# Performance work log

Measured on AMD Instinct MI355X. Metric: run time of the kernel, lower is better.

## Reference

```python
import jax, jax.numpy as jnp
import numpy as np

B, D, C, H = 65536, 256, 128, 1024
SPLIT = D // 2           # transformed half (odd indices under 'even' mask)
NET_IN = (D - SPLIT) + C # unchanged half + cond


def setup_inputs() -> dict:
    key = jax.random.key(0)
    ks = jax.random.split(key, 10)
    s = 0.02
    return {
        "x": jax.random.normal(ks[0], (B, D), jnp.float32),
        "cond": jax.random.normal(ks[1], (B, C), jnp.float32),
        "W1": jax.random.normal(ks[2], (NET_IN, H), jnp.float32) * s,
        "b1": jnp.zeros((H,), jnp.float32),
        "W2": jax.random.normal(ks[3], (H, H), jnp.float32) * s,
        "b2": jnp.zeros((H,), jnp.float32),
        "Ws": jax.random.normal(ks[4], (H, SPLIT), jnp.float32) * s,
        "bs": jnp.zeros((SPLIT,), jnp.float32),
        "Wt": jax.random.normal(ks[5], (H, SPLIT), jnp.float32) * s,
        "bt": jnp.zeros((SPLIT,), jnp.float32),
    }


def reference(x, cond, W1, b1, W2, b2, Ws, bs, Wt, bt):
    d = x.shape[1]
    even = jnp.arange(0, d, 2)  # mask==1 -> unchanged (x1)
    odd = jnp.arange(1, d, 2)   # mask==0 -> transformed (x2)
    x1u = x[:, even]            # (B, d - d//2)
    x2u = x[:, odd]             # (B, d//2)
    h = jax.nn.relu(jnp.concatenate([x1u, cond], axis=1) @ W1 + b1)
    h = jax.nn.relu(h @ W2 + b2)
    log_s = jnp.tanh(h @ Ws + bs)
    t = h @ Wt + bt
    x2t = x2u * jnp.exp(log_s) + t
    out = jnp.zeros_like(x).at[:, even].set(x1u).at[:, odd].set(x2t)
    log_det = jnp.sum(log_s, axis=1)
    return out, log_det
```

## Files before the change

kernel.cpp:

```cpp
#include <hip/hip_runtime.h>
#include <hip/hip_bf16.h>
#include <math.h>

#define B_ROWS 65536
#define D_DIM 256
#define C_DIM 128
#define H_DIM 1024

typedef __bf16 bf16x8 __attribute__((ext_vector_type(8)));
typedef float f32x4 __attribute__((ext_vector_type(4)));
typedef short short8 __attribute__((ext_vector_type(8)));

__device__ __forceinline__ unsigned short f2bf(float f) {
    unsigned int u = __float_as_uint(f);
    u += 0x7fffu + ((u >> 16) & 1u);
    return (unsigned short)(u >> 16);
}

__device__ __forceinline__ void gl2lds16(const void* g, void* l) {
    __builtin_amdgcn_global_load_lds(
        (const __attribute__((address_space(1))) unsigned int*)g,
        (__attribute__((address_space(3))) unsigned int*)l, 16, 0, 0);
}

__device__ __forceinline__ void swizzle_mn(int id, int mtiles, int& m, int& n) {
    if ((mtiles & 7) == 0) {
        int g = id >> 6, r = id & 63;
        m = g * 8 + (r & 7);
        n = r >> 3;
    } else {
        m = id >> 3;
        n = id & 7;
    }
}

__global__ void transpose_bf16(const float* __restrict__ src, short* __restrict__ dst,
                               int R, int C, int total) {
    int tid = blockIdx.x * 256 + threadIdx.x;
    if (tid >= total) return;
    int per = R >> 3;
    int n = tid / per;
    int k0 = (tid - n * per) << 3;
    short8 o;
#pragma unroll
    for (int j = 0; j < 8; ++j) o[j] = (short)f2bf(src[(size_t)(k0 + j) * C + n]);
    *(short8*)&dst[(size_t)n * R + k0] = o;
}

__global__ void prep_b3(const float* __restrict__ bs, const float* __restrict__ bt,
                        float* __restrict__ b3) {
    int i = threadIdx.x;
    b3[i] = (i < 128) ? bs[i] : bt[i - 128];
}

__global__ __launch_bounds__(256) void gemm1_fused(
    const float* __restrict__ x, const float* __restrict__ cond,
    const short* __restrict__ Bw, const float* __restrict__ bias,
    unsigned short* __restrict__ H1, int mtiles) {
    constexpr int BK = 64, K = 256, N = 1024;
    __shared__ __align__(16) short As[128 * BK];
    __shared__ __align__(16) short Bs[128 * BK];
    const int tid = threadIdx.x;
    const int lane = tid & 63;
    const int wave = tid >> 6;
    int mt, nt;
    swizzle_mn(blockIdx.x, mtiles, mt, nt);
    const int tm = mt * 128, tn = nt * 128;
    const int mo = (wave >> 1) * 64;
    const int no = (wave & 1) * 64;

    f32x4 acc[4][4];
#pragma unroll
    for (int i = 0; i < 4; ++i)
#pragma unroll
        for (int j = 0; j < 4; ++j) acc[i][j] = f32x4{0.f, 0.f, 0.f, 0.f};

    const int srow = lane >> 3;
    const int skb = (lane & 7) ^ srow;

#pragma unroll
    for (int kc = 0; kc < K; kc += BK) {
        __syncthreads();
#pragma unroll
        for (int i = 0; i < 4; ++i) {
            int c = wave * 4 + i;
            int row = c * 8 + srow;
            int kcol = kc + skb * 8;
            float v[8];
            if (kc < 128) {
                const float4* p = (const float4*)(x + (size_t)(tm + row) * 256 + 2 * kcol);
                float4 a = p[0], b = p[1], cc = p[2], d = p[3];
                v[0]=a.x; v[1]=a.z; v[2]=b.x; v[3]=b.z; v[4]=cc.x; v[5]=cc.z; v[6]=d.x; v[7]=d.z;
            } else {
                const float4* p = (const float4*)(cond + (size_t)(tm + row) * 128 + (kcol - 128));
                float4 a = p[0], b = p[1];
                v[0]=a.x; v[1]=a.y; v[2]=a.z; v[3]=a.w; v[4]=b.x; v[5]=b.y; v[6]=b.z; v[7]=b.w;
            }
            short8 o;
#pragma unroll
            for (int j = 0; j < 8; ++j) o[j] = (short)f2bf(v[j]);
            *(short8*)&As[c * 512 + lane * 8] = o;
            gl2lds16(Bw + (size_t)(tn + row) * K + kc + skb * 8, &Bs[c * 512]);
        }
        __syncthreads();
#pragma unroll
        for (int kk = 0; kk < 2; ++kk) {
            bf16x8 af[4], bfr[4];
            int kb = kk * 4 + (lane >> 4);
#pragma unroll
            for (int t = 0; t < 4; ++t) {
                int r = mo + t * 16 + (lane & 15);
                af[t] = *(const bf16x8*)&As[r * BK + ((kb ^ (r & 7)) << 3)];
                int n = no + t * 16 + (lane & 15);
                bfr[t] = *(const bf16x8*)&Bs[n * BK + ((kb ^ (n & 7)) << 3)];
            }
#pragma unroll
            for (int i = 0; i < 4; ++i)
#pragma unroll
                for (int j = 0; j < 4; ++j)
                    acc[i][j] = __builtin_amdgcn_mfma_f32_16x16x32_bf16(
                        af[i], bfr[j], acc[i][j], 0, 0, 0);
        }
    }

#pragma unroll
    for (int j = 0; j < 4; ++j) {
        int col = tn + no + j * 16 + (lane & 15);
        float bb = bias[col];
#pragma unroll
        for (int i = 0; i < 4; ++i) {
            int row0 = tm + mo + i * 16 + ((lane >> 4) << 2);
            f32x4 v = acc[i][j];
#pragma unroll
            for (int rr = 0; rr < 4; ++rr)
                H1[(size_t)(row0 + rr) * N + col] = f2bf(fmaxf(v[rr] + bb, 0.f));
        }
    }
}

__global__ __launch_bounds__(256) void gemm_tn(
    const short* __restrict__ A, const short* __restrict__ Bw,
    const float* __restrict__ bias, unsigned short* __restrict__ Cout,
    int mtiles, int N, int K) {
    constexpr int BK = 64;
    __shared__ __align__(16) short As[128 * BK];
    __shared__ __align__(16) short Bs[128 * BK];
    const int tid = threadIdx.x;
    const int lane = tid & 63;
    const int wave = tid >> 6;
    int mt, nt;
    swizzle_mn(blockIdx.x, mtiles, mt, nt);
    const int tm = mt * 128, tn = nt * 128;
    const int mo = (wave >> 1) * 64;
    const int no = (wave & 1) * 64;

    f32x4 acc[4][4];
#pragma unroll
    for (int i = 0; i < 4; ++i)
#pragma unroll
        for (int j = 0; j < 4; ++j) acc[i][j] = f32x4{0.f, 0.f, 0.f, 0.f};

    const int srow = lane >> 3;
    const int skb = (lane & 7) ^ srow;

    for (int kc = 0; kc < K; kc += BK) {
        __syncthreads();
#pragma unroll
        for (int i = 0; i < 4; ++i) {
            int c = wave * 4 + i;
            int row = c * 8 + srow;
            gl2lds16(A + (size_t)(tm + row) * K + kc + skb * 8, &As[c * 512]);
            gl2lds16(Bw + (size_t)(tn + row) * K + kc + skb * 8, &Bs[c * 512]);
        }
        __syncthreads();
#pragma unroll
        for (int kk = 0; kk < 2; ++kk) {
            bf16x8 af[4], bfr[4];
            int kb = kk * 4 + (lane >> 4);
#pragma unroll
            for (int t = 0; t < 4; ++t) {
                int r = mo + t * 16 + (lane & 15);
                af[t] = *(const bf16x8*)&As[r * BK + ((kb ^ (r & 7)) << 3)];
                int n = no + t * 16 + (lane & 15);
                bfr[t] = *(const bf16x8*)&Bs[n * BK + ((kb ^ (n & 7)) << 3)];
            }
#pragma unroll
            for (int i = 0; i < 4; ++i)
#pragma unroll
                for (int j = 0; j < 4; ++j)
                    acc[i][j] = __builtin_amdgcn_mfma_f32_16x16x32_bf16(
                        af[i], bfr[j], acc[i][j], 0, 0, 0);
        }
    }

#pragma unroll
    for (int j = 0; j < 4; ++j) {
        int col = tn + no + j * 16 + (lane & 15);
        float bb = bias[col];
#pragma unroll
        for (int i = 0; i < 4; ++i) {
            int row0 = tm + mo + i * 16 + ((lane >> 4) << 2);
            f32x4 v = acc[i][j];
#pragma unroll
            for (int rr = 0; rr < 4; ++rr)
                Cout[(size_t)(row0 + rr) * N + col] = f2bf(fmaxf(v[rr] + bb, 0.f));
        }
    }
}

__global__ __launch_bounds__(512, 2) void gemm2_8ph(
    const short* __restrict__ A, const short* __restrict__ Bw,
    const float* __restrict__ bias, unsigned short* __restrict__ Cout) {
    constexpr int K = 1024, N = 1024, NT = 16;
    __shared__ __align__(16) short As0[256 * 64];
    __shared__ __align__(16) short Bs0[256 * 64];
    __shared__ __align__(16) short As1[256 * 64];
    __shared__ __align__(16) short Bs1[256 * 64];

    const int tid = threadIdx.x;
    const int lane = tid & 63;
    const int wave = tid >> 6;
    const int wm = wave >> 2;
    const int wn = wave & 3;
    const int l15 = lane & 15;
    const int quad = lane >> 4;
    const int srow = lane >> 3;
    const int skb8 = ((lane & 7) ^ srow) << 3;

    const int id = blockIdx.x, nwg = gridDim.x;
    const int xcd = id & 7, lid = id >> 3;
    const int q = nwg >> 3, r = nwg & 7;
    const int wgid = (xcd < r ? xcd * (q + 1) : r * (q + 1) + (xcd - r) * q) + lid;
    const int mt = wgid >> 2, nt = wgid & 3;
    const size_t Abase = (size_t)(mt * 256) * K;
    const size_t Bbase = (size_t)(nt * 256) * K;

    f32x4 acc[8][4];
#pragma unroll
    for (int m = 0; m < 8; ++m)
#pragma unroll
        for (int n = 0; n < 4; ++n) acc[m][n] = f32x4{0.f, 0.f, 0.f, 0.f};

    short *Ac = As0, *Bc = Bs0, *An = As1, *Bn = Bs1;

    auto stage2 = [&](short* lds, const short* g, size_t rowbase, int kc, int c0, int c1) {
        gl2lds16(g + rowbase + (size_t)(c0 * 8 + srow) * K + kc + skb8, &lds[c0 * 512]);
        gl2lds16(g + rowbase + (size_t)(c1 * 8 + srow) * K + kc + skb8, &lds[c1 * 512]);
    };
    auto stageU = [&](int u, short* Ab, short* Bb, int kc) {
        if (u == 0)      stage2(Bb, Bw, Bbase, kc, wave * 2, wave * 2 + 1);
        else if (u == 1) stage2(Bb, Bw, Bbase, kc, 16 + wave * 2, 17 + wave * 2);
        else if (u == 2) stage2(Ab, A, Abase, kc, wave, 16 + wave);
        else             stage2(Ab, A, Abase, kc, 8 + wave, 24 + wave);
    };

    stageU(0, Ac, Bc, 0);
    stageU(1, Ac, Bc, 0);
    stageU(2, Ac, Bc, 0);
    stageU(3, Ac, Bc, 0);
    stageU(0, An, Bn, 64);
    stageU(1, An, Bn, 64);
    stageU(2, An, Bn, 64);
    asm volatile("s_waitcnt vmcnt(6)" ::: "memory");
    __builtin_amdgcn_sched_barrier(0);
    __builtin_amdgcn_s_barrier();

    for (int w = 0; w < NT; ++w) {
        const int kc1 = (w + 1) << 6, kc2 = (w + 2) << 6;
        bf16x8 bfr[4][2], af[2][2];

#pragma unroll
        for (int n = 0; n < 4; ++n) {
            int rB = (wn << 6) + n * 16 + l15;
#pragma unroll
            for (int kk = 0; kk < 2; ++kk) {
                int kb = kk * 4 + quad;
                bfr[n][kk] = *(const bf16x8*)&Bc[rB * 64 + ((kb ^ (rB & 7)) << 3)];
            }
        }
#pragma unroll
        for (int mm = 0; mm < 2; ++mm) {
            int rA = (wm << 7) + mm * 16 + l15;
#pragma unroll
            for (int kk = 0; kk < 2; ++kk) {
                int kb = kk * 4 + quad;
                af[mm][kk] = *(const bf16x8*)&Ac[rA * 64 + ((kb ^ (rA & 7)) << 3)];
            }
        }
        if (w + 1 < NT) stageU(3, An, Bn, kc1);
        __builtin_amdgcn_sched_barrier(0);
        __builtin_amdgcn_s_barrier();
        __builtin_amdgcn_sched_barrier(0);
        __builtin_amdgcn_s_setprio(1);
#pragma unroll
        for (int kk = 0; kk < 2; ++kk)
#pragma unroll
            for (int mm = 0; mm < 2; ++mm)
#pragma unroll
                for (int n = 0; n < 4; ++n)
                    acc[mm][n] = __builtin_amdgcn_mfma_f32_16x16x32_bf16(
                        af[mm][kk], bfr[n][kk], acc[mm][n], 0, 0, 0);
        __builtin_amdgcn_s_setprio(0);
        __builtin_amdgcn_sched_barrier(0);
        __builtin_amdgcn_s_barrier();

#pragma unroll
        for (int ph = 1; ph < 4; ++ph) {
#pragma unroll
            for (int mm = 0; mm < 2; ++mm) {
                int rA = (wm << 7) + (ph * 2 + mm) * 16 + l15;
#pragma unroll
                for (int kk = 0; kk < 2; ++kk) {
                    int kb = kk * 4 + quad;
                    af[mm][kk] = *(const bf16x8*)&Ac[rA * 64 + ((kb ^ (rA & 7)) << 3)];
                }
            }
            if (w + 2 < NT) stageU(ph - 1, Ac, Bc, kc2);
            __builtin_amdgcn_sched_barrier(0);
            __builtin_amdgcn_s_barrier();
            __builtin_amdgcn_sched_barrier(0);
            __builtin_amdgcn_s_setprio(1);
#pragma unroll
            for (int kk = 0; kk < 2; ++kk)
#pragma unroll
                for (int mm = 0; mm < 2; ++mm)
#pragma unroll
                    for (int n = 0; n < 4; ++n)
                        acc[ph * 2 + mm][n] = __builtin_amdgcn_mfma_f32_16x16x32_bf16(
                            af[mm][kk], bfr[n][kk], acc[ph * 2 + mm][n], 0, 0, 0);
            __builtin_amdgcn_s_setprio(0);
            if (ph == 3) {
                if (w < NT - 2)
                    asm volatile("s_waitcnt vmcnt(6)" ::: "memory");
                else
                    asm volatile("s_waitcnt vmcnt(0)" ::: "memory");
            }
            __builtin_amdgcn_sched_barrier(0);
            __builtin_amdgcn_s_barrier();
        }

        short* t0 = Ac; Ac = An; An = t0;
        short* t1 = Bc; Bc = Bn; Bn = t1;
    }

    const int tmg = mt * 256 + (wm << 7);
    const int tng = nt * 256 + (wn << 6);
#pragma unroll
    for (int n = 0; n < 4; ++n) {
        int col = tng + n * 16 + l15;
        float bb = bias[col];
#pragma unroll
        for (int m = 0; m < 8; ++m) {
            int row0 = tmg + m * 16 + (quad << 2);
            f32x4 v = acc[m][n];
#pragma unroll
            for (int rr = 0; rr < 4; ++rr)
                Cout[(size_t)(row0 + rr) * N + col] = f2bf(fmaxf(v[rr] + bb, 0.f));
        }
    }
}

__global__ __launch_bounds__(256) void gemm3_final(
    const short* __restrict__ H2, const short* __restrict__ W3T,
    const float* __restrict__ b3, const float* __restrict__ x,
    float* __restrict__ out, float* __restrict__ logdet) {
    constexpr int BK = 64, K = 1024;
    __shared__ __align__(16) char raw[40960];
    __shared__ float rowsum[64];
    short* As = (short*)raw;
    short* Bs = (short*)(raw + 8192);
    float* Tbuf = (float*)raw;
    const int tid = threadIdx.x;
    const int lane = tid & 63;
    const int wave = tid >> 6;
    const int tm = blockIdx.x * 64;
    const int srow = lane >> 3;
    const int skb = (lane & 7) ^ srow;
    const int l15 = lane & 15;
    const int quad = lane >> 4;

    if (tid < 64) rowsum[tid] = 0.f;

    f32x4 acc[4][4];
#pragma unroll
    for (int i = 0; i < 4; ++i)
#pragma unroll
        for (int j = 0; j < 4; ++j) acc[i][j] = f32x4{0.f, 0.f, 0.f, 0.f};

    for (int kc = 0; kc < K; kc += BK) {
        __syncthreads();
#pragma unroll
        for (int i = 0; i < 10; ++i) {
            int c = wave * 10 + i;
            if (c < 8) {
                int row = c * 8 + srow;
                gl2lds16(H2 + (size_t)(tm + row) * K + kc + skb * 8, &As[c * 512]);
            } else {
                int row = (c - 8) * 8 + srow;
                gl2lds16(W3T + (size_t)row * K + kc + skb * 8, &Bs[(c - 8) * 512]);
            }
        }
        __syncthreads();
#pragma unroll
        for (int kk = 0; kk < 2; ++kk) {
            int kb = kk * 4 + quad;
            bf16x8 af[4], bfr[4];
#pragma unroll
            for (int mt = 0; mt < 4; ++mt) {
                int r = mt * 16 + l15;
                af[mt] = *(const bf16x8*)&As[r * BK + ((kb ^ (r & 7)) << 3)];
            }
#pragma unroll
            for (int nt = 0; nt < 4; ++nt) {
                int n = wave * 64 + nt * 16 + l15;
                bfr[nt] = *(const bf16x8*)&Bs[n * BK + ((kb ^ (n & 7)) << 3)];
            }
#pragma unroll
            for (int mt = 0; mt < 4; ++mt)
#pragma unroll
                for (int nt = 0; nt < 4; ++nt)
                    acc[mt][nt] = __builtin_amdgcn_mfma_f32_16x16x32_bf16(
                        af[mt], bfr[nt], acc[mt][nt], 0, 0, 0);
        }
    }

    __syncthreads();
    if (wave >= 2) {
#pragma unroll
        for (int nt = 0; nt < 4; ++nt) {
            int col = wave * 64 + nt * 16 + l15;
            float bb = b3[col];
            int cl = col - 128;
#pragma unroll
            for (int mt = 0; mt < 4; ++mt) {
#pragma unroll
                for (int rr = 0; rr < 4; ++rr) {
                    int m = mt * 16 + quad * 4 + rr;
                    Tbuf[m * 132 + cl] = acc[mt][nt][rr] + bb;
                }
            }
        }
    }
    __syncthreads();
    if (wave < 2) {
#pragma unroll
        for (int mt = 0; mt < 4; ++mt) {
#pragma unroll
            for (int rr = 0; rr < 4; ++rr) {
                int m = mt * 16 + quad * 4 + rr;
                int grow = tm + m;
                float s = 0.f;
#pragma unroll
                for (int nt = 0; nt < 4; ++nt) {
                    int j = wave * 64 + nt * 16 + l15;
                    float p = acc[mt][nt][rr] + b3[j];
                    p = fminf(fmaxf(p, -15.f), 15.f);
                    float e2 = __expf(2.f * p);
                    float ls = (e2 - 1.f) / (e2 + 1.f);
                    s += ls;
                    float tt = Tbuf[m * 132 + j];
                    float2 xv = *(const float2*)&x[(size_t)grow * 256 + 2 * j];
                    float2 ov;
                    ov.x = xv.x;
                    ov.y = xv.y * __expf(ls) + tt;
                    *(float2*)&out[(size_t)grow * 256 + 2 * j] = ov;
                }
                s += __shfl_xor(s, 1);
                s += __shfl_xor(s, 2);
                s += __shfl_xor(s, 4);
                s += __shfl_xor(s, 8);
                if (l15 == 0) atomicAdd(&rowsum[m], s);
            }
        }
    }
    __syncthreads();
    if (tid < 64) logdet[tm + tid] = rowsum[tid];
}

extern "C" void kernel_launch(void* const* d_in, const int* in_sizes, int n_in,
                              void* d_out, int out_size, void* d_ws, size_t ws_size,
                              hipStream_t stream) {
    const float* x = (const float*)d_in[0];
    const float* cond = (const float*)d_in[1];
    const float* W1 = (const float*)d_in[2];
    const float* b1 = (const float*)d_in[3];
    const float* W2 = (const float*)d_in[4];
    const float* b2 = (const float*)d_in[5];
    const float* Wsp = (const float*)d_in[6];
    const float* bs = (const float*)d_in[7];
    const float* Wtp = (const float*)d_in[8];
    const float* bt = (const float*)d_in[9];

    char* ws = (char*)d_ws;
    short* W1T = (short*)(ws);
    short* W2T = (short*)(ws + 524288ull);
    short* W3T = (short*)(ws + 2621440ull);
    float* b3  = (float*)(ws + 3145728ull);
    const size_t chunk_base = 3149824ull;

    int n_chunks = 1;
    while (n_chunks < 512) {
        size_t rp = (size_t)B_ROWS / n_chunks;
        if (chunk_base + rp * 4096ull <= ws_size) break;
        n_chunks *= 2;
    }
    const size_t RP = (size_t)B_ROWS / n_chunks;

    float* out = (float*)d_out;
    float* logdet = out + (size_t)B_ROWS * D_DIM;

    transpose_bf16<<<(32768 + 255) / 256, 256, 0, stream>>>(W1, W1T, 256, 1024, 32768);
    transpose_bf16<<<(131072 + 255) / 256, 256, 0, stream>>>(W2, W2T, 1024, 1024, 131072);
    transpose_bf16<<<(16384 + 255) / 256, 256, 0, stream>>>(Wsp, W3T, 1024, 128, 16384);
    transpose_bf16<<<(16384 + 255) / 256, 256, 0, stream>>>(Wtp, W3T + 131072, 1024, 128, 16384);
    prep_b3<<<1, 256, 0, stream>>>(bs, bt, b3);

    for (int c = 0; c < n_chunks; ++c) {
        const size_t r0 = (size_t)c * RP;
        short* H1 = (short*)(ws + chunk_base);
        short* H2 = (short*)(ws + chunk_base + 2048ull * RP);
        const int mtiles = (int)(RP / 128);

        gemm1_fused<<<mtiles * 8, 256, 0, stream>>>(
            x + r0 * D_DIM, cond + r0 * C_DIM, W1T, b1, (unsigned short*)H1, mtiles);
        if ((RP & 255) == 0) {
            gemm2_8ph<<<(int)(RP / 256) * 4, 512, 0, stream>>>(
                H1, W2T, b2, (unsigned short*)H2);
        } else {
            gemm_tn<<<mtiles * 8, 256, 0, stream>>>(
                H1, W2T, b2, (unsigned short*)H2, mtiles, H_DIM, H_DIM);
        }
        gemm3_final<<<(int)(RP / 64), 256, 0, stream>>>(
            H2, W3T, b3, x + r0 * D_DIM, out + r0 * D_DIM, logdet + r0);
    }
}
```

Baseline: 490.7 us.

## Use single LDS buffer with asm ds_reads and coalesced LDS-staged epilogue in gemm2

Replaces the four separate LDS arrays with one buffer addressed by constant offsets, unrolls the loop by two windows so buffer roles are compile-time, and reads fragments with inline-asm ds_read_b128 using precomputed swizzle offsets. Prefetch issue is moved ahead of the LDS reads. The output epilogue now stages the bf16 tile in LDS and writes 16-byte coalesced rows instead of scattered 2-byte stores. The explicit lgkmcnt(0) waits and volatile asm reads may constrain compiler scheduling.

After: 477.3 us. -2.7%, faster.

```diff
diff --git a/kernel.cpp b/kernel.cpp
--- a/kernel.cpp
+++ b/kernel.cpp
@@ -21,6 +21,14 @@
     __builtin_amdgcn_global_load_lds(
         (const __attribute__((address_space(1))) unsigned int*)g,
         (__attribute__((address_space(3))) unsigned int*)l, 16, 0, 0);
+}
+
+__device__ __forceinline__ bf16x8 ds_read_b128_asm(const short* p) {
+    bf16x8 r;
+    asm volatile("ds_read_b128 %0, %1"
+                 : "=v"(r)
+                 : "v"((const __attribute__((address_space(3))) short*)p));
+    return r;
 }
 
 __device__ __forceinline__ void swizzle_mn(int id, int mtiles, int& m, int& n) {
@@ -211,11 +219,9 @@
 __global__ __launch_bounds__(512, 2) void gemm2_8ph(
     const short* __restrict__ A, const short* __restrict__ Bw,
     const float* __restrict__ bias, unsigned short* __restrict__ Cout) {
-    constexpr int K = 1024, N = 1024, NT = 16;
-    __shared__ __align__(16) short As0[256 * 64];
-    __shared__ __align__(16) short Bs0[256 * 64];
-    __shared__ __align__(16) short As1[256 * 64];
-    __shared__ __align__(16) short Bs1[256 * 64];
+    constexpr int K = 1024, NT = 16;
+    constexpr unsigned OFF_A0 = 0, OFF_B0 = 16384, OFF_A1 = 32768, OFF_B1 = 49152;
+    __shared__ __align__(16) short smem[65536];
 
     const int tid = threadIdx.x;
     const int lane = tid & 63;
@@ -241,55 +247,40 @@
 #pragma unroll
         for (int n = 0; n < 4; ++n) acc[m][n] = f32x4{0.f, 0.f, 0.f, 0.f};
 
-    short *Ac = As0, *Bc = Bs0, *An = As1, *Bn = Bs1;
-
-    auto stage2 = [&](short* lds, const short* g, size_t rowbase, int kc, int c0, int c1) {
-        gl2lds16(g + rowbase + (size_t)(c0 * 8 + srow) * K + kc + skb8, &lds[c0 * 512]);
-        gl2lds16(g + rowbase + (size_t)(c1 * 8 + srow) * K + kc + skb8, &lds[c1 * 512]);
+    auto stage2 = [&](unsigned off, const short* g, size_t rowbase, int kc, int c0, int c1) {
+        gl2lds16(g + rowbase + (size_t)(c0 * 8 + srow) * K + kc + skb8, smem + off + c0 * 512);
+        gl2lds16(g + rowbase + (size_t)(c1 * 8 + srow) * K + kc + skb8, smem + off + c1 * 512);
     };
-    auto stageU = [&](int u, short* Ab, short* Bb, int kc) {
-        if (u == 0)      stage2(Bb, Bw, Bbase, kc, wave * 2, wave * 2 + 1);
-        else if (u == 1) stage2(Bb, Bw, Bbase, kc, 16 + wave * 2, 17 + wave * 2);
-        else if (u == 2) stage2(Ab, A, Abase, kc, wave, 16 + wave);
-        else             stage2(Ab, A, Abase, kc, 8 + wave, 24 + wave);
+    auto stageU = [&](int u, unsigned aOff, unsigned bOff, int kc) {
+        if (u == 0)      stage2(bOff, Bw, Bbase, kc, wave * 2, wave * 2 + 1);
+        else if (u == 1) stage2(bOff, Bw, Bbase, kc, 16 + wave * 2, 17 + wave * 2);
+        else if (u == 2) stage2(aOff, A, Abase, kc, wave, 16 + wave);
+        else             stage2(aOff, A, Abase, kc, 8 + wave, 24 + wave);
     };
 
-    stageU(0, Ac, Bc, 0);
-    stageU(1, Ac, Bc, 0);
-    stageU(2, Ac, Bc, 0);
-    stageU(3, Ac, Bc, 0);
-    stageU(0, An, Bn, 64);
-    stageU(1, An, Bn, 64);
-    stageU(2, An, Bn, 64);
-    asm volatile("s_waitcnt vmcnt(6)" ::: "memory");
-    __builtin_amdgcn_sched_barrier(0);
-    __builtin_amdgcn_s_barrier();
-
-    for (int w = 0; w < NT; ++w) {
+    const unsigned x0 = (unsigned)((quad ^ (l15 & 7)) << 3);
+    const unsigned x1 = (unsigned)(((4 + quad) ^ (l15 & 7)) << 3);
+
+    auto window = [&](int w, unsigned caOff, unsigned cbOff, unsigned naOff, unsigned nbOff) {
         const int kc1 = (w + 1) << 6, kc2 = (w + 2) << 6;
+        const short* aA = smem + caOff + ((wm << 7) + l15) * 64;
+        const short* aB = smem + cbOff + ((wn << 6) + l15) * 64;
         bf16x8 bfr[4][2], af[2][2];
 
+        if (w + 1 < NT) stageU(3, naOff, nbOff, kc1);
 #pragma unroll
         for (int n = 0; n < 4; ++n) {
-            int rB = (wn << 6) + n * 16 + l15;
-#pragma unroll
-            for (int kk = 0; kk < 2; ++kk) {
-                int kb = kk * 4 + quad;
-                bfr[n][kk] = *(const bf16x8*)&Bc[rB * 64 + ((kb ^ (rB & 7)) << 3)];
-            }
+            bfr[n][0] = ds_read_b128_asm(aB + n * 1024 + x0);
+            bfr[n][1] = ds_read_b128_asm(aB + n * 1024 + x1);
         }
 #pragma unroll
         for (int mm = 0; mm < 2; ++mm) {
-            int rA = (wm << 7) + mm * 16 + l15;
-#pragma unroll
-            for (int kk = 0; kk < 2; ++kk) {
-                int kb = kk * 4 + quad;
-                af[mm][kk] = *(const bf16x8*)&Ac[rA * 64 + ((kb ^ (rA & 7)) << 3)];
-            }
-        }
-        if (w + 1 < NT) stageU(3, An, Bn, kc1);
+            af[mm][0] = ds_read_b128_asm(aA + mm * 1024 + x0);
+            af[mm][1] = ds_read_b128_asm(aA + mm * 1024 + x1);
+        }
         __builtin_amdgcn_sched_barrier(0);
         __builtin_amdgcn_s_barrier();
+        asm volatile("s_waitcnt lgkmcnt(0)" ::: "memory");
         __builtin_amdgcn_sched_barrier(0);
         __builtin_amdgcn_s_setprio(1);
 #pragma unroll
@@ -306,18 +297,15 @@
 
 #pragma unroll
         for (int ph = 1; ph < 4; ++ph) {
+            if (w + 2 < NT) stageU(ph - 1, caOff, cbOff, kc2);
 #pragma unroll
             for (int mm = 0; mm < 2; ++mm) {
-                int rA = (wm << 7) + (ph * 2 + mm) * 16 + l15;
-#pragma unroll
-                for (int kk = 0; kk < 2; ++kk) {
-                    int kb = kk * 4 + quad;
-                    af[mm][kk] = *(const bf16x8*)&Ac[rA * 64 + ((kb ^ (rA & 7)) << 3)];
-                }
-            }
-            if (w + 2 < NT) stageU(ph - 1, Ac, Bc, kc2);
+                af[mm][0] = ds_read_b128_asm(aA + (ph * 2 + mm) * 1024 + x0);
+                af[mm][1] = ds_read_b128_asm(aA + (ph * 2 + mm) * 1024 + x1);
+            }
             __builtin_amdgcn_sched_barrier(0);
             __builtin_amdgcn_s_barrier();
+            asm volatile("s_waitcnt lgkmcnt(0)" ::: "memory");
             __builtin_amdgcn_sched_barrier(0);
             __builtin_amdgcn_s_setprio(1);
 #pragma unroll
@@ -338,25 +326,47 @@
             __builtin_amdgcn_sched_barrier(0);
             __builtin_amdgcn_s_barrier();
         }
-
-        short* t0 = Ac; Ac = An; An = t0;
-        short* t1 = Bc; Bc = Bn; Bn = t1;
-    }
-
-    const int tmg = mt * 256 + (wm << 7);
-    const int tng = nt * 256 + (wn << 6);
+    };
+
+    stageU(0, OFF_A0, OFF_B0, 0);
+    stageU(1, OFF_A0, OFF_B0, 0);
+    stageU(2, OFF_A0, OFF_B0, 0);
+    stageU(3, OFF_A0, OFF_B0, 0);
+    stageU(0, OFF_A1, OFF_B1, 64);
+    stageU(1, OFF_A1, OFF_B1, 64);
+    stageU(2, OFF_A1, OFF_B1, 64);
+    asm volatile("s_waitcnt vmcnt(6)" ::: "memory");
+    __builtin_amdgcn_sched_barrier(0);
+    __builtin_amdgcn_s_barrier();
+
+#pragma unroll 1
+    for (int w = 0; w < NT; w += 2) {
+        window(w, OFF_A0, OFF_B0, OFF_A1, OFF_B1);
+        window(w + 1, OFF_A1, OFF_B1, OFF_A0, OFF_B0);
+    }
+
+    __syncthreads();
+    unsigned short* cs = (unsigned short*)smem;
 #pragma unroll
     for (int n = 0; n < 4; ++n) {
-        int col = tng + n * 16 + l15;
-        float bb = bias[col];
+        int col = (wn << 6) + n * 16 + l15;
+        float bb = bias[nt * 256 + col];
 #pragma unroll
         for (int m = 0; m < 8; ++m) {
-            int row0 = tmg + m * 16 + (quad << 2);
-            f32x4 v = acc[m][n];
+            int row = (wm << 7) + m * 16 + (quad << 2);
 #pragma unroll
             for (int rr = 0; rr < 4; ++rr)
-                Cout[(size_t)(row0 + rr) * N + col] = f2bf(fmaxf(v[rr] + bb, 0.f));
-        }
+                cs[(row + rr) * 256 + col] = f2bf(fmaxf(acc[m][n][rr] + bb, 0.f));
+        }
+    }
+    __syncthreads();
+    const size_t cbase = (size_t)(mt * 256) * 1024 + nt * 256;
+    const int rloc = tid >> 5, cchunk = tid & 31;
+#pragma unroll
+    for (int rnd = 0; rnd < 16; ++rnd) {
+        int rw = rnd * 16 + rloc;
+        short8 v = *(const short8*)&cs[rw * 256 + cchunk * 8];
+        *(short8*)((unsigned short*)Cout + cbase + (size_t)rw * 1024 + cchunk * 8) = v;
     }
 }
 
```
